# Performance work log

Measured on AMD Instinct MI355X. Metric: run time of the kernel, lower is better.

## Reference

```python
import jax, jax.numpy as jnp
import numpy as np

B, N, C, H, W = 4, 8, 256, 64, 64
SCALE = 2
D = C * SCALE  # embed_dim*scale, head_size with n_heads=1
EPS = 1e-6


def setup_inputs() -> dict:
    key = jax.random.key(0)
    ks = jax.random.split(key, 6)
    sc = lambda k, sh, f: jax.random.normal(k, sh, jnp.float32) * f
    return {
        "q": jax.random.normal(ks[0], (B, C), jnp.float32),
        "c": jax.random.normal(ks[1], (B, N, C, H, W), jnp.float32),
        "g": jnp.ones((C,), jnp.float32),                 # RMSNorm weight
        "Wq": sc(ks[2], (D, C), C ** -0.5),               # proj_q weight
        "Wkv": sc(ks[3], (2 * D, C), C ** -0.5),          # proj_kv weight
        "Wo": sc(ks[4], (C, D), D ** -0.5),               # proj_out weight
        "bo": jnp.zeros((C,), jnp.float32),               # proj_out bias
    }


def reference(q, c, g, Wq, Wkv, Wo, bo):
    # c: [B,N,C,H,W] -> [B,H,W,N,C]
    cp = jnp.transpose(c, (0, 3, 4, 1, 2))
    # RMSNorm over channel dim
    cn = cp * jax.lax.rsqrt(jnp.mean(cp * cp, axis=-1, keepdims=True) + EPS) * g
    # per-pixel, per-token k/v projection: [B,H,W,N,2D]
    kv = jnp.einsum('bhwnc,dc->bhwnd', cn, Wkv)
    k, v = jnp.split(kv, 2, axis=-1)                      # each [B,H,W,N,D]
    qp = q @ Wq.T                                         # [B,D]
    # broadcast single query over spatial grid; softmax over N context tokens
    dots = jnp.einsum('bd,bhwnd->bhwn', qp, k) * (D ** -0.5)
    att = jax.nn.softmax(dots, axis=-1)                   # [B,H,W,N]
    hvec = jnp.einsum('bhwn,bhwnd->bhwd', att, v)         # [B,H,W,D]
    out = hvec @ Wo.T + bo                                # [B,H,W,C]
    return jnp.transpose(out, (0, 3, 1, 2))               # [B,C,H,W]
```

## Files before the change

### kernel.cpp

```cpp
#include <hip/hip_runtime.h>


typedef __attribute__((ext_vector_type(8))) short short8;
typedef __attribute__((ext_vector_type(4))) float floatx4;

static __device__ __forceinline__ short f2bf(float f) {
  unsigned u = __float_as_uint(f);
  u += 0x7fffu + ((u >> 16) & 1u);
  return (short)(u >> 16);
}

__global__ __launch_bounds__(256) void pre_kernel(
    const float* __restrict__ q, const float* __restrict__ g,
    const float* __restrict__ Wq, const float* __restrict__ Wkv,
    const float* __restrict__ Wo, unsigned char* __restrict__ ws) {
  short* WovgB = (short*)ws;
  float* gqk = (float*)(ws + 131072);
  const int blk = blockIdx.x, tid = threadIdx.x;
  if (blk < 64) {
    const int i0 = blk * 4, c = tid;
    float s0 = 0.f, s1 = 0.f, s2 = 0.f, s3 = 0.f;
    #pragma unroll 8
    for (int d = 0; d < 512; ++d) {
      const float wv = Wkv[(512 + d) * 256 + c];
      s0 = fmaf(Wo[(i0 + 0) * 512 + d], wv, s0);
      s1 = fmaf(Wo[(i0 + 1) * 512 + d], wv, s1);
      s2 = fmaf(Wo[(i0 + 2) * 512 + d], wv, s2);
      s3 = fmaf(Wo[(i0 + 3) * 512 + d], wv, s3);
    }
    const float gc = g[c];
    const int sg = c >> 5, q2 = (c >> 3) & 3, jj = c & 7;
    const float sv[4] = {s0, s1, s2, s3};
    #pragma unroll
    for (int ii = 0; ii < 4; ++ii) {
      const int i = i0 + ii, it = i >> 4, m = i & 15;
      WovgB[((((it * 8 + sg) * 4 + q2) * 16) + m) * 8 + jj] = f2bf(sv[ii] * gc);
    }
  } else if (blk < 68) {
    const int b = blk - 64;
    __shared__ float qps[512];
    for (int d = tid; d < 512; d += 256) {
      float s = 0.f;
      #pragma unroll 16
      for (int cc = 0; cc < 256; ++cc)
        s = fmaf(Wq[d * 256 + cc], q[b * 256 + cc], s);
      qps[d] = s;
    }
    __syncthreads();
    const int c = tid;
    float s = 0.f;
    #pragma unroll 16
    for (int d = 0; d < 512; ++d)
      s = fmaf(Wkv[d * 256 + c], qps[d], s);
    gqk[b * 256 + c] = s * g[c] * 0.044194173824159216f;
  }
}

__global__ __launch_bounds__(512) void stats_kernel(
    const float* __restrict__ cin, unsigned char* __restrict__ ws) {
  const float* gqk = (const float*)(ws + 131072);
  float2* stats = (float2*)(ws + 135168);
  const int blk = blockIdx.x, tid = threadIdx.x;
  const int b = blk >> 6, n = (blk >> 3) & 7, pt = blk & 7;
  const int px = pt * 512 + tid;
  const float* cp = cin + (size_t)(b * 8 + n) * 256 * 4096 + px;
  float ssq = 0.f, dt = 0.f;
  #pragma unroll 16
  for (int ch = 0; ch < 256; ++ch) {
    const float v = cp[(size_t)ch * 4096];
    const float gq = gqk[b * 256 + ch];
    ssq = fmaf(v, v, ssq);
    dt = fmaf(v, gq, dt);
  }
  const float invr = rsqrtf(ssq * (1.f / 256.f) + 1e-6f);
  stats[((size_t)(b * 4096 + px)) * 8 + n] = make_float2(dt * invr, invr);
}

__global__ __launch_bounds__(256) void wsum_kernel(
    const float* __restrict__ cin, unsigned char* __restrict__ ws) {
  const float2* stats = (const float2*)(ws + 135168);
  short8* tfrag = (short8*)(ws + 1183744);
  const int blk = blockIdx.x, tid = threadIdx.x;
  const int b = blk >> 8, cg = (blk >> 4) & 15, pt = blk & 15;
  const int px = pt * 256 + tid;

  float d[8], ir[8];
  const float4* sp = (const float4*)(stats + ((size_t)(b * 4096 + px)) * 8);
  #pragma unroll
  for (int k = 0; k < 4; ++k) {
    const float4 v = sp[k];
    d[2 * k] = v.x; ir[2 * k] = v.y; d[2 * k + 1] = v.z; ir[2 * k + 1] = v.w;
  }
  float mx = d[0];
  #pragma unroll
  for (int n = 1; n < 8; ++n) mx = fmaxf(mx, d[n]);
  float wn[8], Z = 0.f;
  #pragma unroll
  for (int n = 0; n < 8; ++n) { wn[n] = __expf(d[n] - mx); Z += wn[n]; }
  const float iZ = 1.f / Z;
  #pragma unroll
  for (int n = 0; n < 8; ++n) wn[n] *= iZ * ir[n];

  float t[16];
  #pragma unroll
  for (int j = 0; j < 16; ++j) t[j] = 0.f;
  const float* cb = cin + ((size_t)(b * 8) * 256 + cg * 16) * 4096 + px;
  #pragma unroll
  for (int n = 0; n < 8; ++n) {
    const float* cp = cb + (size_t)n * 256 * 4096;
    #pragma unroll
    for (int j = 0; j < 16; ++j)
      t[j] = fmaf(wn[n], cp[(size_t)j * 4096], t[j]);
  }

  const int P = px >> 4, m = px & 15, s = cg >> 1;
  #pragma unroll
  for (int qh = 0; qh < 2; ++qh) {
    const int qq = (cg & 1) * 2 + qh;
    short8 pk;
    #pragma unroll
    for (int jj = 0; jj < 8; ++jj) pk[jj] = f2bf(t[qh * 8 + jj]);
    tfrag[(((b * 256 + P) * 8 + s) * 4 + qq) * 16 + m] = pk;
  }
}

__global__ __launch_bounds__(256, 2) void gemm_kernel(
    const float* __restrict__ bo, const unsigned char* __restrict__ ws,
    float* __restrict__ out) {
  const short8* Av = (const short8*)ws;
  const short8* Tv = (const short8*)(ws + 1183744);
  __shared__ short8 tBs[1024];
  const int blk = blockIdx.x, tid = threadIdx.x;
  const int b = blk >> 6, ig = (blk >> 4) & 3, pxg = blk & 15;
  const int lane = tid & 63, w = tid >> 6;
  const int it = ig * 4 + w;
  const int qf = lane >> 4, m = lane & 15;
  floatx4 acc[16];
  #pragma unroll
  for (int nt = 0; nt < 16; ++nt) acc[nt] = (floatx4){0.f, 0.f, 0.f, 0.f};
  #pragma unroll
  for (int s = 0; s < 8; ++s) {
    if (s) __syncthreads();
    #pragma unroll
    for (int k = 0; k < 4; ++k) {
      const int idx = tid + k * 256;
      const int nt = idx >> 6, r = idx & 63;
      tBs[idx] = Tv[(size_t)((b * 256 + pxg * 16 + nt) * 8 + s) * 64 + r];
    }
    __syncthreads();
    const short8 a = Av[((it * 8 + s) * 4 + qf) * 16 + m];
    #pragma unroll
    for (int nt = 0; nt < 16; ++nt)
      acc[nt] = __builtin_amdgcn_mfma_f32_16x16x32_bf16(a, tBs[nt * 64 + lane], acc[nt], 0, 0, 0);
  }
  float* ob = out + (size_t)(b * 256) * 4096 + pxg * 256;
  #pragma unroll
  for (int nt = 0; nt < 16; ++nt)
    #pragma unroll
    for (int r = 0; r < 4; ++r) {
      const int i = it * 16 + qf * 4 + r;
      ob[(size_t)i * 4096 + nt * 16 + m] = acc[nt][r] + bo[i];
    }
}

extern "C" void kernel_launch(void* const* d_in, const int* in_sizes, int n_in,
                              void* d_out, int out_size, void* d_ws, size_t ws_size,
                              hipStream_t stream) {
  const float* q   = (const float*)d_in[0];
  const float* c   = (const float*)d_in[1];
  const float* g   = (const float*)d_in[2];
  const float* Wq  = (const float*)d_in[3];
  const float* Wkv = (const float*)d_in[4];
  const float* Wo  = (const float*)d_in[5];
  const float* bo  = (const float*)d_in[6];
  float* out = (float*)d_out;
  unsigned char* ws = (unsigned char*)d_ws;
  pre_kernel<<<68, 256, 0, stream>>>(q, g, Wq, Wkv, Wo, ws);
  stats_kernel<<<256, 512, 0, stream>>>(c, ws);
  wsum_kernel<<<1024, 256, 0, stream>>>(c, ws);
  gemm_kernel<<<256, 256, 0, stream>>>(bo, ws, out);
}
```

Measured before the change: 276.0 us.

## Split channel reduction across blocks, vectorize loads, move softmax into separate kernel

The stats pass now splits each pixel's 256-channel reduction into four 64-channel partial sums written to the workspace. Each thread handles four pixels with float4 loads, and the launch grows from 256 to 512 blocks. A new small kernel combines the partials and computes the softmax weights scaled by the inverse RMS. The weighted-sum kernel then reads those precomputed weights and also uses float4 loads over four pixels per thread. This aims for more parallelism and wider memory transactions on the bandwidth-bound passes over c, at the cost of an extra launch and extra workspace traffic for the partial sums.

```diff
diff --git a/kernel.cpp b/kernel.cpp
--- a/kernel.cpp
+++ b/kernel.cpp
@@ -56,71 +56,104 @@
   }
 }
 
-__global__ __launch_bounds__(512) void stats_kernel(
+__global__ __launch_bounds__(256) void stats1_kernel(
     const float* __restrict__ cin, unsigned char* __restrict__ ws) {
   const float* gqk = (const float*)(ws + 131072);
-  float2* stats = (float2*)(ws + 135168);
-  const int blk = blockIdx.x, tid = threadIdx.x;
-  const int b = blk >> 6, n = (blk >> 3) & 7, pt = blk & 7;
-  const int px = pt * 512 + tid;
-  const float* cp = cin + (size_t)(b * 8 + n) * 256 * 4096 + px;
-  float ssq = 0.f, dt = 0.f;
-  #pragma unroll 16
-  for (int ch = 0; ch < 256; ++ch) {
-    const float v = cp[(size_t)ch * 4096];
-    const float gq = gqk[b * 256 + ch];
-    ssq = fmaf(v, v, ssq);
-    dt = fmaf(v, gq, dt);
-  }
-  const float invr = rsqrtf(ssq * (1.f / 256.f) + 1e-6f);
-  stats[((size_t)(b * 4096 + px)) * 8 + n] = make_float2(dt * invr, invr);
+  float2* part = (float2*)(ws + 135168);
+  const int blk = blockIdx.x, tid = threadIdx.x;
+  const int chs = blk & 3, pxt = (blk >> 2) & 3, n = (blk >> 4) & 7, b = blk >> 7;
+  const int px = pxt * 1024 + tid * 4;
+  const float* cp = cin + ((size_t)(b * 8 + n) * 256 + chs * 64) * 4096 + px;
+  const float* gq = gqk + b * 256 + chs * 64;
+  floatx4 ssq = {0.f, 0.f, 0.f, 0.f}, dt = {0.f, 0.f, 0.f, 0.f};
+  #pragma unroll 8
+  for (int ch = 0; ch < 64; ++ch) {
+    const floatx4 v = *(const floatx4*)(cp + (size_t)ch * 4096);
+    const float gg = gq[ch];
+    ssq += v * v;
+    dt += v * gg;
+  }
+  float2* pp = part + ((size_t)((b * 8 + n) * 4 + chs)) * 4096 + px;
+  const floatx4 o0 = {ssq[0], dt[0], ssq[1], dt[1]};
+  const floatx4 o1 = {ssq[2], dt[2], ssq[3], dt[3]};
+  *(floatx4*)pp = o0;
+  *(floatx4*)(pp + 2) = o1;
+}
+
+__global__ __launch_bounds__(128) void stats2_kernel(unsigned char* __restrict__ ws) {
+  const float2* part = (const float2*)(ws + 135168);
+  float* wout = (float*)(ws + 4329472);
+  const int gid = blockIdx.x * 128 + threadIdx.x;
+  const int b = gid >> 12, px = gid & 4095;
+  float dv[8], ir[8];
+  #pragma unroll
+  for (int n = 0; n < 8; ++n) {
+    float ss = 0.f, dd = 0.f;
+    #pragma unroll
+    for (int chs = 0; chs < 4; ++chs) {
+      const float2 pr = part[((size_t)((b * 8 + n) * 4 + chs)) * 4096 + px];
+      ss += pr.x; dd += pr.y;
+    }
+    const float invr = rsqrtf(ss * (1.f / 256.f) + 1e-6f);
+    ir[n] = invr;
+    dv[n] = dd * invr;
+  }
+  float mx = dv[0];
+  #pragma unroll
+  for (int n = 1; n < 8; ++n) mx = fmaxf(mx, dv[n]);
+  float e[8], Z = 0.f;
+  #pragma unroll
+  for (int n = 0; n < 8; ++n) { e[n] = __expf(dv[n] - mx); Z += e[n]; }
+  const float iZ = 1.f / Z;
+  float* wp = wout + ((size_t)(b * 4096 + px)) * 8;
+  #pragma unroll
+  for (int n = 0; n < 8; ++n) wp[n] = e[n] * iZ * ir[n];
 }
 
 __global__ __launch_bounds__(256) void wsum_kernel(
     const float* __restrict__ cin, unsigned char* __restrict__ ws) {
-  const float2* stats = (const float2*)(ws + 135168);
-  short8* tfrag = (short8*)(ws + 1183744);
-  const int blk = blockIdx.x, tid = threadIdx.x;
-  const int b = blk >> 8, cg = (blk >> 4) & 15, pt = blk & 15;
-  const int px = pt * 256 + tid;
-
-  float d[8], ir[8];
-  const float4* sp = (const float4*)(stats + ((size_t)(b * 4096 + px)) * 8);
-  #pragma unroll
-  for (int k = 0; k < 4; ++k) {
-    const float4 v = sp[k];
-    d[2 * k] = v.x; ir[2 * k] = v.y; d[2 * k + 1] = v.z; ir[2 * k + 1] = v.w;
-  }
-  float mx = d[0];
-  #pragma unroll
-  for (int n = 1; n < 8; ++n) mx = fmaxf(mx, d[n]);
-  float wn[8], Z = 0.f;
-  #pragma unroll
-  for (int n = 0; n < 8; ++n) { wn[n] = __expf(d[n] - mx); Z += wn[n]; }
-  const float iZ = 1.f / Z;
-  #pragma unroll
-  for (int n = 0; n < 8; ++n) wn[n] *= iZ * ir[n];
-
-  float t[16];
-  #pragma unroll
-  for (int j = 0; j < 16; ++j) t[j] = 0.f;
-  const float* cb = cin + ((size_t)(b * 8) * 256 + cg * 16) * 4096 + px;
+  const float* wv = (const float*)(ws + 4329472);
+  short8* tfrag = (short8*)(ws + 4853760);
+  const int blk = blockIdx.x, tid = threadIdx.x;
+  const int pxt = blk & 3, cg = (blk >> 2) & 31, b = blk >> 7;
+  const int px = pxt * 1024 + tid * 4;
+
+  float w[4][8];
+  const float* wp = wv + ((size_t)(b * 4096 + px)) * 8;
+  #pragma unroll
+  for (int p = 0; p < 4; ++p) {
+    const floatx4 a = *(const floatx4*)(wp + p * 8);
+    const floatx4 bq = *(const floatx4*)(wp + p * 8 + 4);
+    w[p][0] = a[0]; w[p][1] = a[1]; w[p][2] = a[2]; w[p][3] = a[3];
+    w[p][4] = bq[0]; w[p][5] = bq[1]; w[p][6] = bq[2]; w[p][7] = bq[3];
+  }
+
+  float t[8][4];
+  #pragma unroll
+  for (int j = 0; j < 8; ++j)
+    #pragma unroll
+    for (int p = 0; p < 4; ++p) t[j][p] = 0.f;
+
+  const float* cb = cin + ((size_t)(b * 8) * 256 + cg * 8) * 4096 + px;
   #pragma unroll
   for (int n = 0; n < 8; ++n) {
     const float* cp = cb + (size_t)n * 256 * 4096;
     #pragma unroll
-    for (int j = 0; j < 16; ++j)
-      t[j] = fmaf(wn[n], cp[(size_t)j * 4096], t[j]);
-  }
-
-  const int P = px >> 4, m = px & 15, s = cg >> 1;
-  #pragma unroll
-  for (int qh = 0; qh < 2; ++qh) {
-    const int qq = (cg & 1) * 2 + qh;
+    for (int j = 0; j < 8; ++j) {
+      const floatx4 v = *(const floatx4*)(cp + (size_t)j * 4096);
+      #pragma unroll
+      for (int p = 0; p < 4; ++p) t[j][p] = fmaf(w[p][n], v[p], t[j][p]);
+    }
+  }
+
+  const int P = px >> 4, m = px & 15, s = cg >> 2, qq = cg & 3;
+  short8* tp = tfrag + (((size_t)(b * 256 + P) * 8 + s) * 4 + qq) * 16 + m;
+  #pragma unroll
+  for (int p = 0; p < 4; ++p) {
     short8 pk;
     #pragma unroll
-    for (int jj = 0; jj < 8; ++jj) pk[jj] = f2bf(t[qh * 8 + jj]);
-    tfrag[(((b * 256 + P) * 8 + s) * 4 + qq) * 16 + m] = pk;
+    for (int j = 0; j < 8; ++j) pk[j] = f2bf(t[j][p]);
+    tp[p] = pk;
   }
 }
 
@@ -128,7 +161,7 @@
     const float* __restrict__ bo, const unsigned char* __restrict__ ws,
     float* __restrict__ out) {
   const short8* Av = (const short8*)ws;
-  const short8* Tv = (const short8*)(ws + 1183744);
+  const short8* Tv = (const short8*)(ws + 4853760);
   __shared__ short8 tBs[1024];
   const int blk = blockIdx.x, tid = threadIdx.x;
   const int b = blk >> 6, ig = (blk >> 4) & 3, pxg = blk & 15;
@@ -176,7 +209,8 @@
   float* out = (float*)d_out;
   unsigned char* ws = (unsigned char*)d_ws;
   pre_kernel<<<68, 256, 0, stream>>>(q, g, Wq, Wkv, Wo, ws);
-  stats_kernel<<<256, 512, 0, stream>>>(c, ws);
-  wsum_kernel<<<1024, 256, 0, stream>>>(c, ws);
+  stats1_kernel<<<512, 256, 0, stream>>>(c, ws);
+  stats2_kernel<<<128, 128, 0, stream>>>(ws);
+  wsum_kernel<<<512, 256, 0, stream>>>(c, ws);
   gemm_kernel<<<256, 256, 0, stream>>>(bo, ws, out);
 }
```

Result: slower. 283.9 us (+2.9%).
